# Optimization experiments

Measured on AMD Instinct MI355X. Metric: run time of the kernel, lower is better.

Reference implementation:

```python
import jax, jax.numpy as jnp
import numpy as np

COMMITMENT_COST = 0.25
EPS = 1e-10


def setup_inputs() -> dict:
    key = jax.random.key(0)
    k1, k2 = jax.random.split(key)
    z_e = jax.random.normal(k1, (64, 4096, 64), dtype=jnp.float32)
    codebook = jax.random.normal(k2, (1024, 64), dtype=jnp.float32)
    return {"z_e": z_e, "codebook": codebook}


def reference(z_e, codebook):
    K, d = codebook.shape
    z_flat = z_e.reshape(-1, d)                      # [N, d]
    N = z_flat.shape[0]
    # squared L2 distances: ||z||^2 + ||e||^2 - 2 z.e  -> [N, K]
    distances = (jnp.sum(z_flat ** 2, axis=1, keepdims=True)
                 + jnp.sum(codebook ** 2, axis=1)
                 - 2.0 * jnp.matmul(z_flat, codebook.T))
    idx = jnp.argmin(distances, axis=1)              # [N]
    # direct gather (equivalent to one-hot @ codebook)
    z_q_flat = codebook[idx]                         # [N, d]
    z_q = z_q_flat.reshape(z_e.shape)
    e_latent_loss = jnp.mean((jax.lax.stop_gradient(z_q) - z_e) ** 2)
    q_latent_loss = jnp.mean((z_q - jax.lax.stop_gradient(z_e)) ** 2)
    loss = q_latent_loss + COMMITMENT_COST * e_latent_loss
    # avg one-hot probs via scatter-add (counts / N)
    counts = jnp.zeros((K,), dtype=jnp.float32).at[idx].add(1.0)
    avg_probs = counts / N
    perplexity = jnp.exp(-jnp.sum(avg_probs * jnp.log(avg_probs + EPS)))
    # straight-through estimator
    z_q_st = z_e + jax.lax.stop_gradient(z_q - z_e)
    return (z_q_st, loss, perplexity)
```

## Files before the change

### kernel.cpp

```cpp
#include <hip/hip_runtime.h>
#include <math.h>

#define NROWS   (64 * 4096)
#define D       64
#define K       1024
#define NELEM   ((size_t)NROWS * (size_t)D)

#define CHUNK_CODES 128
#define ROWB        144
#define NRM_OFF     (CHUNK_CODES * ROWB)
#define REC_USED    (NRM_OFF + 512)
#define REC_BYTES   20480
#define NCHUNK      (K / CHUNK_CODES)
#define WS_CHUNK_OFF 16384
#define WS_MAIN_NEED (WS_CHUNK_OFF + NCHUNK * REC_BYTES)
#define BLK_ROWS    256
#define NBLOCKS     (NROWS / BLK_ROWS)

#define MBIAS  256.0f
#define GAP_Q  0.4f

typedef float  f32x4  __attribute__((ext_vector_type(4)));
typedef short  s16x8  __attribute__((ext_vector_type(8)));


static __device__ inline unsigned bf16_rne(unsigned u) {
  return (u + 0x7FFFu + ((u >> 16) & 1u)) >> 16;
}
static __device__ inline unsigned umin_(unsigned a, unsigned b) { return a < b ? a : b; }
static __device__ inline unsigned umax_(unsigned a, unsigned b) { return a > b ? a : b; }

__global__ __launch_bounds__(256) void vq_prep(const float* __restrict__ cb,
                                               char* __restrict__ ws) {
  int k = blockIdx.x * 256 + threadIdx.x;
  if (k >= K) return;
  int chunk = k >> 7, cc = k & 127;
  char* rec = ws + WS_CHUNK_OFF + chunk * REC_BYTES;
  unsigned short* hrow = (unsigned short*)(rec + cc * ROWB);
  const float* src = cb + (k << 6);
  float nrm = 0.f;
  for (int j = 0; j < 64; j += 2) {
    float x0 = src[j], x1 = src[j + 1];
    nrm = fmaf(x0, x0, fmaf(x1, x1, nrm));
    unsigned h0 = bf16_rne(__float_as_uint(x0));
    unsigned h1 = bf16_rne(__float_as_uint(x1));
    *(unsigned*)(hrow + j) = h0 | (h1 << 16);
  }
  *(float*)(rec + NRM_OFF + cc * 4) = nrm + MBIAS;
}

__global__ __launch_bounds__(256, 4) void vq_mfma(const float* __restrict__ z,
                                                  const float* __restrict__ cb,
                                                  const char* __restrict__ ws,
                                                  float* __restrict__ zq,
                                                  unsigned int* __restrict__ counts,
                                                  float* __restrict__ block_loss) {
  __shared__ __align__(16) char sblob[REC_BYTES];

  const int t    = threadIdx.x;
  const int w    = t >> 6;
  const int lane = t & 63;
  const int g    = lane >> 4;
  const int ln16 = lane & 15;

  const int rowbase = blockIdx.x * BLK_ROWS + w * 64;
  s16x8 zh[4][2];
#pragma unroll
  for (int rt = 0; rt < 4; ++rt) {
    int row = rowbase + rt * 16 + ln16;
    const float4* zr = (const float4*)(z + (size_t)row * 64);
#pragma unroll
    for (int ks = 0; ks < 2; ++ks) {
      float4 a = zr[ks * 8 + g * 2];
      float4 b = zr[ks * 8 + g * 2 + 1];
      s16x8 hh;
      hh[0] = (short)bf16_rne(__float_as_uint(a.x));
      hh[1] = (short)bf16_rne(__float_as_uint(a.y));
      hh[2] = (short)bf16_rne(__float_as_uint(a.z));
      hh[3] = (short)bf16_rne(__float_as_uint(a.w));
      hh[4] = (short)bf16_rne(__float_as_uint(b.x));
      hh[5] = (short)bf16_rne(__float_as_uint(b.y));
      hh[6] = (short)bf16_rne(__float_as_uint(b.z));
      hh[7] = (short)bf16_rne(__float_as_uint(b.w));
      zh[rt][ks] = hh;
    }
  }

  unsigned q1[4] = {~0u, ~0u, ~0u, ~0u};
  unsigned q2[4] = {~0u, ~0u, ~0u, ~0u};
  unsigned q3[4] = {~0u, ~0u, ~0u, ~0u};

  const int aoff = ln16 * ROWB + g * 16;

#define LD_TILE(TL, E0, E1, NR) {                                             \
    const char* _ab = sblob + (TL) * (16 * ROWB) + aoff;                      \
    E0 = *(const s16x8*)(_ab);                                                \
    E1 = *(const s16x8*)(_ab + 64);                                           \
    NR = *(const f32x4*)(sblob + NRM_OFF + (TL) * 64 + (g << 4)); }

  for (int c = 0; c < NCHUNK; ++c) {
    __syncthreads();
    {
      const float4* src = (const float4*)(ws + WS_CHUNK_OFF + c * REC_BYTES);
      float4* dst = (float4*)sblob;
#pragma unroll
      for (int i = 0; i < 5; ++i) {
        int idx = t + 256 * i;
        dst[idx] = src[idx];
      }
    }
    __syncthreads();

    s16x8 e0a, e1a; f32x4 nra;
    LD_TILE(0, e0a, e1a, nra)
#pragma unroll
    for (int tl = 0; tl < 8; ++tl) {
      s16x8 e0b, e1b; f32x4 nrb;
      if (tl < 7) { LD_TILE(tl + 1, e0b, e1b, nrb) }

      f32x4 ac0 = {0.f,0.f,0.f,0.f}, ac1 = {0.f,0.f,0.f,0.f};
      f32x4 ac2 = {0.f,0.f,0.f,0.f}, ac3 = {0.f,0.f,0.f,0.f};
      ac0 = __builtin_amdgcn_mfma_f32_16x16x32_bf16(e0a, zh[0][0], ac0, 0, 0, 0);
      ac1 = __builtin_amdgcn_mfma_f32_16x16x32_bf16(e0a, zh[1][0], ac1, 0, 0, 0);
      ac2 = __builtin_amdgcn_mfma_f32_16x16x32_bf16(e0a, zh[2][0], ac2, 0, 0, 0);
      ac3 = __builtin_amdgcn_mfma_f32_16x16x32_bf16(e0a, zh[3][0], ac3, 0, 0, 0);
      ac0 = __builtin_amdgcn_mfma_f32_16x16x32_bf16(e1a, zh[0][1], ac0, 0, 0, 0);
      ac1 = __builtin_amdgcn_mfma_f32_16x16x32_bf16(e1a, zh[1][1], ac1, 0, 0, 0);
      ac2 = __builtin_amdgcn_mfma_f32_16x16x32_bf16(e1a, zh[2][1], ac2, 0, 0, 0);
      ac3 = __builtin_amdgcn_mfma_f32_16x16x32_bf16(e1a, zh[3][1], ac3, 0, 0, 0);

      const unsigned kb = (unsigned)((c << 7) + (tl << 4) + (g << 2));
#define UPDP(RT, R) {                                                         \
        float m = fmaf(-2.f, ac##RT[R], nra[R]);                              \
        unsigned key = (__float_as_uint(m) & 0xFFFFFC00u) | (kb + R);         \
        unsigned t1 = umax_(q1[RT], key); q1[RT] = umin_(q1[RT], key);        \
        unsigned t2 = umax_(q2[RT], t1);  q2[RT] = umin_(q2[RT], t1);         \
        q3[RT] = umin_(q3[RT], t2); }
      UPDP(0, 0) UPDP(1, 0) UPDP(2, 0) UPDP(3, 0)
      UPDP(0, 1) UPDP(1, 1) UPDP(2, 1) UPDP(3, 1)
      UPDP(0, 2) UPDP(1, 2) UPDP(2, 2) UPDP(3, 2)
      UPDP(0, 3) UPDP(1, 3) UPDP(2, 3) UPDP(3, 3)
#undef UPDP
      if (tl < 7) { e0a = e0b; e1a = e1b; nra = nrb; }
    }
  }

  __syncthreads();
  int*   sk  = (int*)sblob;
  float* red = (float*)(sblob + 1024);

  const float4* cb4 = (const float4*)cb;
  const float4* z4g = (const float4*)z;

#pragma unroll
  for (int rt = 0; rt < 4; ++rt) {
    unsigned a1 = q1[rt], a2 = q2[rt], a3 = q3[rt];
#pragma unroll
    for (int dx = 16; dx <= 32; dx <<= 1) {
      unsigned b1 = (unsigned)__shfl_xor((int)a1, dx);
      unsigned b2 = (unsigned)__shfl_xor((int)a2, dx);
      unsigned b3 = (unsigned)__shfl_xor((int)a3, dx);
      unsigned x  = umax_(a1, b1);
      a1 = umin_(a1, b1);
      unsigned y  = umin_(a2, b2);
      unsigned zz = umax_(a2, b2);
      unsigned w3 = umin_(a3, b3);
      a2 = umin_(x, y);
      a3 = umin_(umax_(x, y), umin_(zz, w3));
    }
    int   i1 = (int)(a1 & 1023u), i2 = (int)(a2 & 1023u);
    float f1 = __uint_as_float(a1 & 0xFFFFFC00u);
    float f2 = __uint_as_float(a2 & 0xFFFFFC00u);
    float f3 = __uint_as_float(a3 & 0xFFFFFC00u);
    bool needFull = (f3 - f1) < GAP_Q;
    bool needPair = !needFull && ((f2 - f1) < GAP_Q);
    int  kstar = i1;

    if (g == 0) {
      int row = rowbase + rt * 16 + ln16;
      if (needPair) {
        float d1 = 0.f, d2 = 0.f;
        const float4* zr = z4g + (size_t)row * 16;
        const float4* c1 = cb4 + i1 * 16;
        const float4* c2 = cb4 + i2 * 16;
#pragma unroll
        for (int j = 0; j < 16; ++j) {
          float4 zv = zr[j], a = c1[j], b = c2[j];
          float e;
          e = zv.x - a.x; d1 = fmaf(e, e, d1);
          e = zv.y - a.y; d1 = fmaf(e, e, d1);
          e = zv.z - a.z; d1 = fmaf(e, e, d1);
          e = zv.w - a.w; d1 = fmaf(e, e, d1);
          e = zv.x - b.x; d2 = fmaf(e, e, d2);
          e = zv.y - b.y; d2 = fmaf(e, e, d2);
          e = zv.z - b.z; d2 = fmaf(e, e, d2);
          e = zv.w - b.w; d2 = fmaf(e, e, d2);
        }
        if (d2 < d1 || (d2 == d1 && i2 < i1)) kstar = i2;
      }
      if (!needFull) {
        sk[w * 64 + rt * 16 + ln16] = kstar;
        atomicAdd(&counts[kstar], 1u);
      }
    }

    unsigned long long fullmask = __ballot(needFull && g == 0);
    while (fullmask) {
      int src = __ffsll(fullmask) - 1;
      fullmask &= fullmask - 1;
      int lrow = w * 64 + rt * 16 + src;
      int row  = blockIdx.x * BLK_ROWS + lrow;
      const float4* zr = z4g + (size_t)row * 16;
      float bv = 3.4e38f; int bi = 0;
      for (int c16 = 0; c16 < 16; ++c16) {
        int code = c16 * 64 + lane;
        const float4* cr = cb4 + code * 16;
        float d = 0.f;
#pragma unroll
        for (int j = 0; j < 16; ++j) {
          float4 zv = zr[j], cv = cr[j];
          float e;
          e = zv.x - cv.x; d = fmaf(e, e, d);
          e = zv.y - cv.y; d = fmaf(e, e, d);
          e = zv.z - cv.z; d = fmaf(e, e, d);
          e = zv.w - cv.w; d = fmaf(e, e, d);
        }
        if (d < bv) { bv = d; bi = code; }
      }
#pragma unroll
      for (int dx = 1; dx < 64; dx <<= 1) {
        float ov = __shfl_xor(bv, dx); int oi = __shfl_xor(bi, dx);
        if (ov < bv || (ov == bv && oi < bi)) { bv = ov; bi = oi; }
      }
      if (lane == 0) { sk[lrow] = bi; atomicAdd(&counts[bi], 1u); }
    }
  }

  __syncthreads();

  float lpart = 0.f;
  const int base4 = blockIdx.x * (BLK_ROWS * 16);
  float4* out4 = (float4*)zq;
#pragma unroll
  for (int i = 0; i < 16; ++i) {
    int idx = t + 256 * i;
    int row = idx >> 4, c4 = idx & 15;
    int kk = sk[row];
    float4 cv = cb4[kk * 16 + c4];
    float4 zv = z4g[base4 + idx];
    float e;
    e = zv.x - cv.x; lpart = fmaf(e, e, lpart);
    e = zv.y - cv.y; lpart = fmaf(e, e, lpart);
    e = zv.z - cv.z; lpart = fmaf(e, e, lpart);
    e = zv.w - cv.w; lpart = fmaf(e, e, lpart);
    out4[base4 + idx] = cv;
  }
  red[t] = lpart;
  __syncthreads();
#pragma unroll
  for (int s = 128; s > 0; s >>= 1) {
    if (t < s) red[t] += red[t + s];
    __syncthreads();
  }
  if (t == 0) block_loss[blockIdx.x] = red[0];
}

__global__ __launch_bounds__(1024) void vq_finalize(const unsigned int* __restrict__ counts,
                                                    const float* __restrict__ block_loss,
                                                    float* __restrict__ out, int nb) {
  __shared__ float sh[1024];
  __shared__ float sl[1024];
  const int t = threadIdx.x;
  float c = (float)counts[t];
  float p = c * (1.0f / (float)NROWS);
  sh[t] = p * logf(p + 1e-10f);
  float bl = (t < nb) ? block_loss[t] : 0.f;
  sl[t] = bl;
  __syncthreads();
#pragma unroll
  for (int s = 512; s > 0; s >>= 1) {
    if (t < s) { sh[t] += sh[t + s]; sl[t] += sl[t + s]; }
    __syncthreads();
  }
  if (t == 0) {
    out[NELEM]     = 1.25f * sl[0] / (float)NELEM;
    out[NELEM + 1] = expf(-sh[0]);
  }
}

#define DOT4(acc, a, e) \
  acc = fmaf((a).x, (e).x, fmaf((a).y, (e).y, fmaf((a).z, (e).z, fmaf((a).w, (e).w, (acc)))))
#define SQD4(acc, a, e) { \
  float _dx = (e).x - (a).x, _dy = (e).y - (a).y, _dz = (e).z - (a).z, _dw = (e).w - (a).w; \
  acc = fmaf(_dx, _dx, fmaf(_dy, _dy, fmaf(_dz, _dz, fmaf(_dw, _dw, (acc))))); }

__global__ __launch_bounds__(256) void vq_norms_fb(const float* __restrict__ cb,
                                                   float* __restrict__ norms) {
  int k = blockIdx.x * blockDim.x + threadIdx.x;
  if (k >= K) return;
  const float4* e4 = (const float4*)(cb + (k << 6));
  float a0 = 0.f, a1 = 0.f, a2 = 0.f, a3 = 0.f;
#pragma unroll
  for (int j = 0; j < 16; j += 4) {
    float4 e;
    e = e4[j + 0]; DOT4(a0, e, e);
    e = e4[j + 1]; DOT4(a1, e, e);
    e = e4[j + 2]; DOT4(a2, e, e);
    e = e4[j + 3]; DOT4(a3, e, e);
  }
  norms[k] = (a0 + a1) + (a2 + a3);
}

__global__ __launch_bounds__(256) void vq_main_fb(const float* __restrict__ z,
                                                  const float* __restrict__ cb,
                                                  const float* __restrict__ norms,
                                                  float* __restrict__ zq,
                                                  unsigned int* __restrict__ counts,
                                                  float* __restrict__ block_loss) {
  const int tid = threadIdx.x;
  const int row = blockIdx.x * 256 + tid;
  const float4* zr4 = (const float4*)(z + (size_t)row * D);
  float4 zr[16];
#pragma unroll
  for (int j = 0; j < 16; ++j) zr[j] = zr4[j];
  float best = 3.4e38f;
  int   bidx = 0;
  for (int k = 0; k < K; k += 2) {
    const float4* e0 = (const float4*)(cb + (k << 6));
    const float4* e1 = e0 + 16;
    float a0 = 0.f, a1 = 0.f, a2 = 0.f, a3 = 0.f;
    float b0 = 0.f, b1 = 0.f, b2 = 0.f, b3 = 0.f;
#pragma unroll
    for (int j = 0; j < 16; j += 4) {
      float4 tt;
      tt = e0[j + 0]; DOT4(a0, zr[j + 0], tt);
      tt = e1[j + 0]; DOT4(b0, zr[j + 0], tt);
      tt = e0[j + 1]; DOT4(a1, zr[j + 1], tt);
      tt = e1[j + 1]; DOT4(b1, zr[j + 1], tt);
      tt = e0[j + 2]; DOT4(a2, zr[j + 2], tt);
      tt = e1[j + 2]; DOT4(b2, zr[j + 2], tt);
      tt = e0[j + 3]; DOT4(a3, zr[j + 3], tt);
      tt = e1[j + 3]; DOT4(b3, zr[j + 3], tt);
    }
    float d0 = (a0 + a1) + (a2 + a3);
    float d1 = (b0 + b1) + (b2 + b3);
    float m0 = fmaf(-2.f, d0, norms[k]);
    float m1 = fmaf(-2.f, d1, norms[k + 1]);
    if (m0 < best) { best = m0; bidx = k; }
    if (m1 < best) { best = m1; bidx = k + 1; }
  }
  const float4* eb4 = (const float4*)(cb + ((size_t)bidx << 6));
  float4* o4 = (float4*)(zq + (size_t)row * D);
  float l0 = 0.f, l1 = 0.f, l2 = 0.f, l3 = 0.f;
#pragma unroll
  for (int j = 0; j < 16; j += 4) {
    float4 e;
    e = eb4[j + 0]; o4[j + 0] = e; SQD4(l0, zr[j + 0], e);
    e = eb4[j + 1]; o4[j + 1] = e; SQD4(l1, zr[j + 1], e);
    e = eb4[j + 2]; o4[j + 2] = e; SQD4(l2, zr[j + 2], e);
    e = eb4[j + 3]; o4[j + 3] = e; SQD4(l3, zr[j + 3], e);
  }
  float row_loss = (l0 + l1) + (l2 + l3);
  atomicAdd(&counts[bidx], 1u);
  __shared__ float redf[256];
  redf[tid] = row_loss;
  __syncthreads();
#pragma unroll
  for (int s = 128; s > 0; s >>= 1) {
    if (tid < s) redf[tid] += redf[tid + s];
    __syncthreads();
  }
  if (tid == 0) block_loss[blockIdx.x] = redf[0];
}

extern "C" void kernel_launch(void* const* d_in, const int* in_sizes, int n_in,
                              void* d_out, int out_size, void* d_ws, size_t ws_size,
                              hipStream_t stream) {
  const float* z  = (const float*)d_in[0];
  const float* cb = (const float*)d_in[1];
  float* out = (float*)d_out;

  unsigned int* counts     = (unsigned int*)d_ws;
  float*        block_loss = (float*)((char*)d_ws + 4096);

  hipMemsetAsync(d_ws, 0, 4096, stream);

  if (ws_size >= WS_MAIN_NEED) {
    vq_prep<<<dim3(4), dim3(256), 0, stream>>>(cb, (char*)d_ws);
    vq_mfma<<<dim3(NBLOCKS), dim3(256), 0, stream>>>(z, cb, (const char*)d_ws,
                                                     out, counts, block_loss);
    vq_finalize<<<dim3(1), dim3(1024), 0, stream>>>(counts, block_loss, out, NBLOCKS);
  } else {
    float* norms = (float*)((char*)d_ws + 12288);
    vq_norms_fb<<<dim3(4), dim3(256), 0, stream>>>(cb, norms);
    vq_main_fb<<<dim3(NROWS / 256), dim3(256), 0, stream>>>(z, cb, norms,
                                                            out, counts, block_loss);
    vq_finalize<<<dim3(1), dim3(1024), 0, stream>>>(counts, block_loss, out, 1024);
  }
}
```

Measured before the change: 246.0 us.

## Fold -2 scale and norm bias into MFMA accumulator, stage 256 codes per phase

The prep kernel now stores bf16 codebook rows pre-scaled by -2 and keeps the norms in a separate array. The main kernel seeds the MFMA accumulators with the norm+bias, so the per-element fma in the top-3 update disappears. Codes are staged in 256-code phases (4 LDS fills instead of 8), and two 16-code tiles are processed per iteration for more independent MFMAs. The cost is more LDS per block (about 37.9 KB), which may reduce occupancy. Scaling by -2 before rounding shifts where bf16 rounding error lands, and the candidate-gap threshold GAP_Q is raised to 0.8, presumably to send more near-ties to the exact recheck.

```diff
diff --git a/kernel.cpp b/kernel.cpp
--- a/kernel.cpp
+++ b/kernel.cpp
@@ -6,19 +6,20 @@
 #define K       1024
 #define NELEM   ((size_t)NROWS * (size_t)D)
 
-#define CHUNK_CODES 128
 #define ROWB        144
-#define NRM_OFF     (CHUNK_CODES * ROWB)
-#define REC_USED    (NRM_OFF + 512)
-#define REC_BYTES   20480
-#define NCHUNK      (K / CHUNK_CODES)
+#define CODES_BYTES (K * ROWB)
 #define WS_CHUNK_OFF 16384
-#define WS_MAIN_NEED (WS_CHUNK_OFF + NCHUNK * REC_BYTES)
+#define WS_MAIN_NEED (WS_CHUNK_OFF + CODES_BYTES + K * 4)
+#define PH_CODES    256
+#define PH_CBYTES   (PH_CODES * ROWB)
+#define LDS_NRM_OFF PH_CBYTES
+#define LDS_BYTES   (PH_CBYTES + PH_CODES * 4)
+#define NPHASE      (K / PH_CODES)
 #define BLK_ROWS    256
 #define NBLOCKS     (NROWS / BLK_ROWS)
 
 #define MBIAS  256.0f
-#define GAP_Q  0.4f
+#define GAP_Q  0.8f
 
 typedef float  f32x4  __attribute__((ext_vector_type(4)));
 typedef short  s16x8  __attribute__((ext_vector_type(8)));
@@ -34,19 +35,17 @@
                                                char* __restrict__ ws) {
   int k = blockIdx.x * 256 + threadIdx.x;
   if (k >= K) return;
-  int chunk = k >> 7, cc = k & 127;
-  char* rec = ws + WS_CHUNK_OFF + chunk * REC_BYTES;
-  unsigned short* hrow = (unsigned short*)(rec + cc * ROWB);
+  unsigned short* hrow = (unsigned short*)(ws + WS_CHUNK_OFF + k * ROWB);
   const float* src = cb + (k << 6);
   float nrm = 0.f;
   for (int j = 0; j < 64; j += 2) {
     float x0 = src[j], x1 = src[j + 1];
     nrm = fmaf(x0, x0, fmaf(x1, x1, nrm));
-    unsigned h0 = bf16_rne(__float_as_uint(x0));
-    unsigned h1 = bf16_rne(__float_as_uint(x1));
+    unsigned h0 = bf16_rne(__float_as_uint(-2.f * x0));
+    unsigned h1 = bf16_rne(__float_as_uint(-2.f * x1));
     *(unsigned*)(hrow + j) = h0 | (h1 << 16);
   }
-  *(float*)(rec + NRM_OFF + cc * 4) = nrm + MBIAS;
+  *(float*)(ws + WS_CHUNK_OFF + CODES_BYTES + k * 4) = nrm + MBIAS;
 }
 
 __global__ __launch_bounds__(256, 4) void vq_mfma(const float* __restrict__ z,
@@ -55,7 +54,7 @@
                                                   float* __restrict__ zq,
                                                   unsigned int* __restrict__ counts,
                                                   float* __restrict__ block_loss) {
-  __shared__ __align__(16) char sblob[REC_BYTES];
+  __shared__ __align__(16) char sblob[LDS_BYTES];
 
   const int t    = threadIdx.x;
   const int w    = t >> 6;
@@ -92,56 +91,66 @@
 
   const int aoff = ln16 * ROWB + g * 16;
 
-#define LD_TILE(TL, E0, E1, NR) {                                             \
-    const char* _ab = sblob + (TL) * (16 * ROWB) + aoff;                      \
-    E0 = *(const s16x8*)(_ab);                                                \
-    E1 = *(const s16x8*)(_ab + 64);                                           \
-    NR = *(const f32x4*)(sblob + NRM_OFF + (TL) * 64 + (g << 4)); }
-
-  for (int c = 0; c < NCHUNK; ++c) {
+  for (int p = 0; p < NPHASE; ++p) {
     __syncthreads();
     {
-      const float4* src = (const float4*)(ws + WS_CHUNK_OFF + c * REC_BYTES);
+      const float4* csrc = (const float4*)(ws + WS_CHUNK_OFF + (size_t)p * PH_CBYTES);
       float4* dst = (float4*)sblob;
 #pragma unroll
-      for (int i = 0; i < 5; ++i) {
-        int idx = t + 256 * i;
-        dst[idx] = src[idx];
-      }
+      for (int i = 0; i < 9; ++i)
+        dst[t + 256 * i] = csrc[t + 256 * i];
+      if (t < 64)
+        ((float4*)(sblob + LDS_NRM_OFF))[t] =
+            ((const float4*)(ws + WS_CHUNK_OFF + CODES_BYTES + (size_t)p * 1024))[t];
     }
     __syncthreads();
 
-    s16x8 e0a, e1a; f32x4 nra;
-    LD_TILE(0, e0a, e1a, nra)
-#pragma unroll
-    for (int tl = 0; tl < 8; ++tl) {
-      s16x8 e0b, e1b; f32x4 nrb;
-      if (tl < 7) { LD_TILE(tl + 1, e0b, e1b, nrb) }
-
-      f32x4 ac0 = {0.f,0.f,0.f,0.f}, ac1 = {0.f,0.f,0.f,0.f};
-      f32x4 ac2 = {0.f,0.f,0.f,0.f}, ac3 = {0.f,0.f,0.f,0.f};
-      ac0 = __builtin_amdgcn_mfma_f32_16x16x32_bf16(e0a, zh[0][0], ac0, 0, 0, 0);
-      ac1 = __builtin_amdgcn_mfma_f32_16x16x32_bf16(e0a, zh[1][0], ac1, 0, 0, 0);
-      ac2 = __builtin_amdgcn_mfma_f32_16x16x32_bf16(e0a, zh[2][0], ac2, 0, 0, 0);
-      ac3 = __builtin_amdgcn_mfma_f32_16x16x32_bf16(e0a, zh[3][0], ac3, 0, 0, 0);
-      ac0 = __builtin_amdgcn_mfma_f32_16x16x32_bf16(e1a, zh[0][1], ac0, 0, 0, 0);
-      ac1 = __builtin_amdgcn_mfma_f32_16x16x32_bf16(e1a, zh[1][1], ac1, 0, 0, 0);
-      ac2 = __builtin_amdgcn_mfma_f32_16x16x32_bf16(e1a, zh[2][1], ac2, 0, 0, 0);
-      ac3 = __builtin_amdgcn_mfma_f32_16x16x32_bf16(e1a, zh[3][1], ac3, 0, 0, 0);
-
-      const unsigned kb = (unsigned)((c << 7) + (tl << 4) + (g << 2));
-#define UPDP(RT, R) {                                                         \
-        float m = fmaf(-2.f, ac##RT[R], nra[R]);                              \
-        unsigned key = (__float_as_uint(m) & 0xFFFFFC00u) | (kb + R);         \
+#pragma unroll 2
+    for (int tl = 0; tl < 16; tl += 2) {
+      const char* abA = sblob + tl * (16 * ROWB) + aoff;
+      const char* abB = abA + 16 * ROWB;
+      s16x8 eA0 = *(const s16x8*)(abA);
+      s16x8 eA1 = *(const s16x8*)(abA + 64);
+      s16x8 eB0 = *(const s16x8*)(abB);
+      s16x8 eB1 = *(const s16x8*)(abB + 64);
+      f32x4 nrA = *(const f32x4*)(sblob + LDS_NRM_OFF + tl * 64 + (g << 4));
+      f32x4 nrB = *(const f32x4*)(sblob + LDS_NRM_OFF + (tl + 1) * 64 + (g << 4));
+
+      f32x4 aA0 = nrA, aA1 = nrA, aA2 = nrA, aA3 = nrA;
+      f32x4 aB0 = nrB, aB1 = nrB, aB2 = nrB, aB3 = nrB;
+      aA0 = __builtin_amdgcn_mfma_f32_16x16x32_bf16(eA0, zh[0][0], aA0, 0, 0, 0);
+      aA1 = __builtin_amdgcn_mfma_f32_16x16x32_bf16(eA0, zh[1][0], aA1, 0, 0, 0);
+      aA2 = __builtin_amdgcn_mfma_f32_16x16x32_bf16(eA0, zh[2][0], aA2, 0, 0, 0);
+      aA3 = __builtin_amdgcn_mfma_f32_16x16x32_bf16(eA0, zh[3][0], aA3, 0, 0, 0);
+      aB0 = __builtin_amdgcn_mfma_f32_16x16x32_bf16(eB0, zh[0][0], aB0, 0, 0, 0);
+      aB1 = __builtin_amdgcn_mfma_f32_16x16x32_bf16(eB0, zh[1][0], aB1, 0, 0, 0);
+      aB2 = __builtin_amdgcn_mfma_f32_16x16x32_bf16(eB0, zh[2][0], aB2, 0, 0, 0);
+      aB3 = __builtin_amdgcn_mfma_f32_16x16x32_bf16(eB0, zh[3][0], aB3, 0, 0, 0);
+      aA0 = __builtin_amdgcn_mfma_f32_16x16x32_bf16(eA1, zh[0][1], aA0, 0, 0, 0);
+      aA1 = __builtin_amdgcn_mfma_f32_16x16x32_bf16(eA1, zh[1][1], aA1, 0, 0, 0);
+      aA2 = __builtin_amdgcn_mfma_f32_16x16x32_bf16(eA1, zh[2][1], aA2, 0, 0, 0);
+      aA3 = __builtin_amdgcn_mfma_f32_16x16x32_bf16(eA1, zh[3][1], aA3, 0, 0, 0);
+      aB0 = __builtin_amdgcn_mfma_f32_16x16x32_bf16(eB1, zh[0][1], aB0, 0, 0, 0);
+      aB1 = __builtin_amdgcn_mfma_f32_16x16x32_bf16(eB1, zh[1][1], aB1, 0, 0, 0);
+      aB2 = __builtin_amdgcn_mfma_f32_16x16x32_bf16(eB1, zh[2][1], aB2, 0, 0, 0);
+      aB3 = __builtin_amdgcn_mfma_f32_16x16x32_bf16(eB1, zh[3][1], aB3, 0, 0, 0);
+
+      const unsigned kbA = (unsigned)(p * PH_CODES + (tl << 4) + (g << 2));
+      const unsigned kbB = kbA + 16;
+#define UPDP(AC, KB, RT, R) {                                                 \
+        unsigned key = (__float_as_uint(AC##RT[R]) & 0xFFFFFC00u) | (KB + R); \
         unsigned t1 = umax_(q1[RT], key); q1[RT] = umin_(q1[RT], key);        \
         unsigned t2 = umax_(q2[RT], t1);  q2[RT] = umin_(q2[RT], t1);         \
         q3[RT] = umin_(q3[RT], t2); }
-      UPDP(0, 0) UPDP(1, 0) UPDP(2, 0) UPDP(3, 0)
-      UPDP(0, 1) UPDP(1, 1) UPDP(2, 1) UPDP(3, 1)
-      UPDP(0, 2) UPDP(1, 2) UPDP(2, 2) UPDP(3, 2)
-      UPDP(0, 3) UPDP(1, 3) UPDP(2, 3) UPDP(3, 3)
+      UPDP(aA, kbA, 0, 0) UPDP(aA, kbA, 1, 0) UPDP(aA, kbA, 2, 0) UPDP(aA, kbA, 3, 0)
+      UPDP(aB, kbB, 0, 0) UPDP(aB, kbB, 1, 0) UPDP(aB, kbB, 2, 0) UPDP(aB, kbB, 3, 0)
+      UPDP(aA, kbA, 0, 1) UPDP(aA, kbA, 1, 1) UPDP(aA, kbA, 2, 1) UPDP(aA, kbA, 3, 1)
+      UPDP(aB, kbB, 0, 1) UPDP(aB, kbB, 1, 1) UPDP(aB, kbB, 2, 1) UPDP(aB, kbB, 3, 1)
+      UPDP(aA, kbA, 0, 2) UPDP(aA, kbA, 1, 2) UPDP(aA, kbA, 2, 2) UPDP(aA, kbA, 3, 2)
+      UPDP(aB, kbB, 0, 2) UPDP(aB, kbB, 1, 2) UPDP(aB, kbB, 2, 2) UPDP(aB, kbB, 3, 2)
+      UPDP(aA, kbA, 0, 3) UPDP(aA, kbA, 1, 3) UPDP(aA, kbA, 2, 3) UPDP(aA, kbA, 3, 3)
+      UPDP(aB, kbB, 0, 3) UPDP(aB, kbB, 1, 3) UPDP(aB, kbB, 2, 3) UPDP(aB, kbB, 3, 3)
 #undef UPDP
-      if (tl < 7) { e0a = e0b; e1a = e1b; nra = nrb; }
     }
   }
 
```

Result: slower. 367.9 us (+49.5%).
